# Performance work log

Hardware: AMD Instinct MI355X
Metric: run time of the kernel (lower is better)

Reference implementation:

```python
import jax, jax.numpy as jnp
import numpy as np

KERNEL_SIZE = 16


def make_directional_kernels(k: int) -> jnp.ndarray:
    """Binary line kernels [4,1,k,k] in order (north, south, east, west),
    matching the stack order in the torch module."""
    half = k // 2
    mid = (k - 1) // 2
    w = np.zeros((4, 1, k, k), dtype=np.float32)
    w[0, 0, :half, mid] = 1.0   # north: top half of center column
    w[1, 0, half:, mid] = 1.0   # south: bottom half of center column
    w[2, 0, mid, half:] = 1.0   # east:  right half of center row
    w[3, 0, mid, :half] = 1.0   # west:  left half of center row
    return jnp.asarray(w)


def setup_inputs() -> dict:
    key = jax.random.key(0)
    k1, k2, k3 = jax.random.split(key, 3)
    x = jax.random.normal(k1, (64, 1, 512, 512), dtype=jnp.float32)
    logits = jax.random.normal(k2, (1, 4), dtype=jnp.float32)
    gumbel_noise = jax.random.normal(k3, (1, 4), dtype=jnp.float32)
    return {"x": x, "logits": logits, "gumbel_noise": gumbel_noise}


def reference(x, logits, gumbel_noise):
    # gumbel-softmax probs (tau=1, hard=False): softmax(logits + G)
    probs = jax.nn.softmax(logits + gumbel_noise, axis=-1)[0]  # [4]
    w = make_directional_kernels(KERNEL_SIZE)                  # [4,1,k,k]
    # One conv producing all 4 directional blurs: [B,4,H,W].
    # Torch padding='same' with even k pads (lo=(k-1)//2, hi=k//2), identical
    # to lax 'SAME' for stride 1.
    motions = jax.lax.conv_general_dilated(
        x, w, window_strides=(1, 1), padding="SAME",
        dimension_numbers=("NCHW", "OIHW", "NCHW"))
    # weighted combine: sum_i probs[i] * motion_i -> [B,1,H,W]
    out = jnp.einsum("bdhw,d->bhw", motions, probs)[:, None, :, :]
    return out
```

## Files before the change

kernel.cpp:

```cpp
#include <hip/hip_runtime.h>
#include <math.h>


#define IMG   512
#define IMG4  128

static __device__ __forceinline__ float4 f4z() {
    return make_float4(0.f, 0.f, 0.f, 0.f);
}

__global__ __launch_bounds__(64, 4) void motion_blur_kernel(
    const float* __restrict__ x,
    const float* __restrict__ logits,
    const float* __restrict__ gnoise,
    float* __restrict__ out)
{
    const int lane = threadIdx.x & 63;

    const int bid  = blockIdx.x;
    const int lbid = (bid & 7) * 1024 + (bid >> 3);

    const int img  = lbid >> 7;
    const int rem  = lbid & 127;
    const int ct   = rem >> 6;
    const int y0   = (rem & 63) * 8;
    const int c4t  = ct * 64;
    const int c4   = c4t + lane;

    float l0 = logits[0] + gnoise[0];
    float l1 = logits[1] + gnoise[1];
    float l2 = logits[2] + gnoise[2];
    float l3 = logits[3] + gnoise[3];
    float mx = fmaxf(fmaxf(l0, l1), fmaxf(l2, l3));
    float e0 = expf(l0 - mx), e1 = expf(l1 - mx);
    float e2 = expf(l2 - mx), e3 = expf(l3 - mx);
    float inv = 1.0f / (e0 + e1 + e2 + e3);
    const float p0  = e0 * inv;
    const float p1  = e1 * inv;
    const float p2  = e2 * inv;
    const float p3  = e3 * inv;
    const float q32 = p3 - p2;
    const float np3 = -p3;

    const float4* __restrict__ xi4 =
        reinterpret_cast<const float4*>(x) + (size_t)img * (IMG * IMG4);

    const int  hc4   = c4t + ((lane < 2) ? (lane - 2) : (lane + 2));
    const bool hlane = (lane < 2) || (lane >= 62);
    const bool hok   = hlane && ((unsigned)hc4 < (unsigned)IMG4);

    const int lm2 = (lane - 2) & 63;
    const int lm1 = (lane - 1) & 63;
    const int lp1 = (lane + 1) & 63;
    const int lp2 = (lane + 2) & 63;

    float4 fifo[16];
    #pragma unroll
    for (int k = 0; k < 16; ++k) {
        const int r = y0 - 7 + k;
        float4 v = f4z();
        if ((unsigned)r < (unsigned)IMG) v = xi4[r * IMG4 + c4];
        fifo[(9 + k) & 15] = v;
    }
    float4 VA = f4z(), VB = f4z();
    #pragma unroll
    for (int k = 0; k < 8; ++k) {
        const float4 v = fifo[(9 + k) & 15];
        VA.x += v.x; VA.y += v.y; VA.z += v.z; VA.w += v.w;
    }
    #pragma unroll
    for (int k = 0; k < 8; ++k) {
        const float4 v = fifo[(1 + k) & 15];
        VB.x += v.x; VB.y += v.y; VB.z += v.z; VB.w += v.w;
    }

    float4 pre[4];
    #pragma unroll
    for (int k = 0; k < 4; ++k) {
        const int r = y0 + 9 + k;
        float4 v = f4z();
        if (r < IMG) v = xi4[r * IMG4 + c4];
        pre[k] = v;
    }

    float4 hv_cur = f4z();
    if (hok) hv_cur = xi4[y0 * IMG4 + hc4];

    float* __restrict__ obase =
        out + (size_t)img * (IMG * IMG) + (size_t)y0 * IMG + 4 * c4;

    #pragma unroll
    for (int i = 0; i < 8; ++i) {
        __builtin_amdgcn_sched_barrier(0x7);

        float4 hv_next = f4z();
        if (i < 7 && hok) hv_next = xi4[(y0 + i + 1) * IMG4 + hc4];

        const float4 cur = fifo[i & 15];
        const float L0 = cur.x;
        const float L1 = L0 + cur.y;
        const float L2 = L1 + cur.z;
        const float L3 = L2 + cur.w;
        const float hL0 = hv_cur.x;
        const float hL1 = hL0 + hv_cur.y;
        const float hL2 = hL1 + hv_cur.z;
        const float hL3 = hL2 + hv_cur.w;

        float Lm0 = __shfl(L0, lm2), Lm1 = __shfl(L1, lm2),
              Lm2_ = __shfl(L2, lm2), Lm3 = __shfl(L3, lm2);
        if (lane < 2) { Lm0 = hL0; Lm1 = hL1; Lm2_ = hL2; Lm3 = hL3; }
        float Lp0 = __shfl(L0, lp2), Lp1 = __shfl(L1, lp2),
              Lp2_ = __shfl(L2, lp2), Lp3 = __shfl(L3, lp2);
        if (lane >= 62) { Lp0 = hL0; Lp1 = hL1; Lp2_ = hL2; Lp3 = hL3; }
        float sm1 = __shfl(L3, lm1);
        const float sm1h = __shfl(hL3, 1);
        if (lane == 0) sm1 = sm1h;
        float sp1 = __shfl(L3, lp1);
        const float sp1h = __shfl(hL3, 62);
        if (lane == 63) sp1 = sp1h;

        const float base = p3 * (Lm3 + sm1) + p2 * (L3 + sp1);
        float4 r4;
        r4.x = fmaf(p0, VA.x, fmaf(p1, VB.x,
                 fmaf(q32, L0, fmaf(np3, Lm0, fmaf(p2, Lp0, base)))));
        r4.y = fmaf(p0, VA.y, fmaf(p1, VB.y,
                 fmaf(q32, L1, fmaf(np3, Lm1, fmaf(p2, Lp1, base)))));
        r4.z = fmaf(p0, VA.z, fmaf(p1, VB.z,
                 fmaf(q32, L2, fmaf(np3, Lm2_, fmaf(p2, Lp2_, base)))));
        r4.w = fmaf(p0, VA.w, fmaf(p1, VB.w,
                 fmaf(q32, L3, fmaf(np3, Lm3, fmaf(p2, Lp3, base)))));
        *reinterpret_cast<float4*>(obase + (size_t)i * IMG) = r4;

        if (i < 7) {
            const float4 vnew = pre[i & 3];
            const float4 a = fifo[(i + 1) & 15];
            const float4 b = fifo[(i + 9) & 15];
            VA.x += a.x - b.x; VA.y += a.y - b.y;
            VA.z += a.z - b.z; VA.w += a.w - b.w;
            VB.x += vnew.x - a.x; VB.y += vnew.y - a.y;
            VB.z += vnew.z - a.z; VB.w += vnew.w - a.w;
            fifo[(i + 9) & 15] = vnew;
            if (i <= 2) {
                const int r = y0 + 13 + i;
                float4 v = f4z();
                if (r < IMG) v = xi4[r * IMG4 + c4];
                pre[i & 3] = v;
            }
        }
        hv_cur = hv_next;
    }
}

extern "C" void kernel_launch(void* const* d_in, const int* in_sizes, int n_in,
                              void* d_out, int out_size, void* d_ws, size_t ws_size,
                              hipStream_t stream) {
    const float* x      = (const float*)d_in[0];
    const float* logits = (const float*)d_in[1];
    const float* gn     = (const float*)d_in[2];
    float* outp         = (float*)d_out;
    motion_blur_kernel<<<dim3(8192), dim3(64), 0, stream>>>(x, logits, gn, outp);
}
```

Baseline: 31.89 us.

## Issue all row loads up front and gather halo columns in one load

Loads all 23 input rows per lane into registers at kernel start instead of streaming them through a FIFO with prefetch. Halo columns for all 8 output rows are fetched by a single cooperative load across 32 lanes and then distributed with shuffles, replacing the per-row halo loads. The aim is to raise memory-level parallelism and remove the serialized reload chain. In exchange register pressure rises, so launch bounds drop from 4 to 3 waves per EU, which may lower occupancy.

New measurement: 29.63 us. -7.1%, faster.

```diff
diff --git a/kernel.cpp b/kernel.cpp
--- a/kernel.cpp
+++ b/kernel.cpp
@@ -9,7 +9,7 @@
     return make_float4(0.f, 0.f, 0.f, 0.f);
 }
 
-__global__ __launch_bounds__(64, 4) void motion_blur_kernel(
+__global__ __launch_bounds__(64, 3) void motion_blur_kernel(
     const float* __restrict__ x,
     const float* __restrict__ logits,
     const float* __restrict__ gnoise,
@@ -27,6 +27,25 @@
     const int c4t  = ct * 64;
     const int c4   = c4t + lane;
 
+    const float4* __restrict__ xi4 =
+        reinterpret_cast<const float4*>(x) + (size_t)img * (IMG * IMG4);
+
+    const int hb   = lane & 3;
+    const int hc4  = c4t + ((hb < 2) ? (hb - 2) : (62 + hb));
+    const int hrow = y0 + (lane >> 2);
+    float4 hq = f4z();
+    if (lane < 32 && (unsigned)hc4 < (unsigned)IMG4)
+        hq = xi4[hrow * IMG4 + hc4];
+
+    float4 v[23];
+    #pragma unroll
+    for (int k = 0; k < 23; ++k) {
+        const int r = y0 - 7 + k;
+        float4 t = f4z();
+        if ((unsigned)r < (unsigned)IMG) t = xi4[r * IMG4 + c4];
+        v[k] = t;
+    }
+
     float l0 = logits[0] + gnoise[0];
     float l1 = logits[1] + gnoise[1];
     float l2 = logits[2] + gnoise[2];
@@ -42,81 +61,56 @@
     const float q32 = p3 - p2;
     const float np3 = -p3;
 
-    const float4* __restrict__ xi4 =
-        reinterpret_cast<const float4*>(x) + (size_t)img * (IMG * IMG4);
+    const float hP0 = hq.x;
+    const float hP1 = hP0 + hq.y;
+    const float hP2 = hP1 + hq.z;
+    const float hP3 = hP2 + hq.w;
 
-    const int  hc4   = c4t + ((lane < 2) ? (lane - 2) : (lane + 2));
-    const bool hlane = (lane < 2) || (lane >= 62);
-    const bool hok   = hlane && ((unsigned)hc4 < (unsigned)IMG4);
+    float4 VA = f4z(), VB = f4z();
+    #pragma unroll
+    for (int k = 0; k < 8; ++k) {
+        VA.x += v[k].x; VA.y += v[k].y; VA.z += v[k].z; VA.w += v[k].w;
+    }
+    #pragma unroll
+    for (int k = 8; k < 16; ++k) {
+        VB.x += v[k].x; VB.y += v[k].y; VB.z += v[k].z; VB.w += v[k].w;
+    }
 
     const int lm2 = (lane - 2) & 63;
     const int lm1 = (lane - 1) & 63;
     const int lp1 = (lane + 1) & 63;
     const int lp2 = (lane + 2) & 63;
-
-    float4 fifo[16];
-    #pragma unroll
-    for (int k = 0; k < 16; ++k) {
-        const int r = y0 - 7 + k;
-        float4 v = f4z();
-        if ((unsigned)r < (unsigned)IMG) v = xi4[r * IMG4 + c4];
-        fifo[(9 + k) & 15] = v;
-    }
-    float4 VA = f4z(), VB = f4z();
-    #pragma unroll
-    for (int k = 0; k < 8; ++k) {
-        const float4 v = fifo[(9 + k) & 15];
-        VA.x += v.x; VA.y += v.y; VA.z += v.z; VA.w += v.w;
-    }
-    #pragma unroll
-    for (int k = 0; k < 8; ++k) {
-        const float4 v = fifo[(1 + k) & 15];
-        VB.x += v.x; VB.y += v.y; VB.z += v.z; VB.w += v.w;
-    }
-
-    float4 pre[4];
-    #pragma unroll
-    for (int k = 0; k < 4; ++k) {
-        const int r = y0 + 9 + k;
-        float4 v = f4z();
-        if (r < IMG) v = xi4[r * IMG4 + c4];
-        pre[k] = v;
-    }
-
-    float4 hv_cur = f4z();
-    if (hok) hv_cur = xi4[y0 * IMG4 + hc4];
+    const int hbase = (lane < 2) ? lane : (lane - 60);
 
     float* __restrict__ obase =
         out + (size_t)img * (IMG * IMG) + (size_t)y0 * IMG + 4 * c4;
 
     #pragma unroll
     for (int i = 0; i < 8; ++i) {
-        __builtin_amdgcn_sched_barrier(0x7);
-
-        float4 hv_next = f4z();
-        if (i < 7 && hok) hv_next = xi4[(y0 + i + 1) * IMG4 + hc4];
-
-        const float4 cur = fifo[i & 15];
+        const float4 cur = v[7 + i];
         const float L0 = cur.x;
         const float L1 = L0 + cur.y;
         const float L2 = L1 + cur.z;
         const float L3 = L2 + cur.w;
-        const float hL0 = hv_cur.x;
-        const float hL1 = hL0 + hv_cur.y;
-        const float hL2 = hL1 + hv_cur.z;
-        const float hL3 = hL2 + hv_cur.w;
 
         float Lm0 = __shfl(L0, lm2), Lm1 = __shfl(L1, lm2),
               Lm2_ = __shfl(L2, lm2), Lm3 = __shfl(L3, lm2);
-        if (lane < 2) { Lm0 = hL0; Lm1 = hL1; Lm2_ = hL2; Lm3 = hL3; }
         float Lp0 = __shfl(L0, lp2), Lp1 = __shfl(L1, lp2),
               Lp2_ = __shfl(L2, lp2), Lp3 = __shfl(L3, lp2);
-        if (lane >= 62) { Lp0 = hL0; Lp1 = hL1; Lp2_ = hL2; Lp3 = hL3; }
+
+        const int hsrc = 4 * i + hbase;
+        const float hV0 = __shfl(hP0, hsrc);
+        const float hV1 = __shfl(hP1, hsrc);
+        const float hV2 = __shfl(hP2, hsrc);
+        const float hV3 = __shfl(hP3, hsrc);
+        if (lane < 2)   { Lm0 = hV0; Lm1 = hV1; Lm2_ = hV2; Lm3 = hV3; }
+        if (lane >= 62) { Lp0 = hV0; Lp1 = hV1; Lp2_ = hV2; Lp3 = hV3; }
+
         float sm1 = __shfl(L3, lm1);
-        const float sm1h = __shfl(hL3, 1);
+        const float sm1h = __shfl(hP3, 4 * i + 1);
         if (lane == 0) sm1 = sm1h;
         float sp1 = __shfl(L3, lp1);
-        const float sp1h = __shfl(hL3, 62);
+        const float sp1h = __shfl(hP3, 4 * i + 2);
         if (lane == 63) sp1 = sp1h;
 
         const float base = p3 * (Lm3 + sm1) + p2 * (L3 + sp1);
@@ -132,22 +126,14 @@
         *reinterpret_cast<float4*>(obase + (size_t)i * IMG) = r4;
 
         if (i < 7) {
-            const float4 vnew = pre[i & 3];
-            const float4 a = fifo[(i + 1) & 15];
-            const float4 b = fifo[(i + 9) & 15];
+            const float4 a = v[8 + i];
+            const float4 b = v[i];
+            const float4 n = v[16 + i];
             VA.x += a.x - b.x; VA.y += a.y - b.y;
             VA.z += a.z - b.z; VA.w += a.w - b.w;
-            VB.x += vnew.x - a.x; VB.y += vnew.y - a.y;
-            VB.z += vnew.z - a.z; VB.w += vnew.w - a.w;
-            fifo[(i + 9) & 15] = vnew;
-            if (i <= 2) {
-                const int r = y0 + 13 + i;
-                float4 v = f4z();
-                if (r < IMG) v = xi4[r * IMG4 + c4];
-                pre[i & 3] = v;
-            }
+            VB.x += n.x - a.x; VB.y += n.y - a.y;
+            VB.z += n.z - a.z; VB.w += n.w - a.w;
         }
-        hv_cur = hv_next;
     }
 }
 
```
